# Optimization experiments

Hardware: AMD Instinct MI355X
Metric: run time of the kernel (lower is better)

## Reference

```python
import jax, jax.numpy as jnp
import numpy as np

# anchor encoding indices: [x,y,z,log w,log l,log h,sin,cos,vx,vy,vz]
NUM_HEADS = 8
LN_EPS = 1e-5


def layer_norm(x, g, b):
    mu = jnp.mean(x, axis=-1, keepdims=True)
    var = jnp.var(x, axis=-1, keepdims=True)
    return (x - mu) * jax.lax.rsqrt(var + LN_EPS) * g + b


def align_anchors_to_frame(anchor, Tm):
    # anchor: (..., N, 11), Tm: (..., 4, 4)
    R = Tm[..., :3, :3]
    t = Tm[..., :3, 3]
    center = jnp.einsum('...ij,...nj->...ni', R, anchor[..., 0:3]) + t[..., None, :]
    size = anchor[..., 3:6]
    yaw = jnp.einsum('...ij,...nj->...ni', R[..., :2, :2], anchor[..., 6:8])
    vel = jnp.einsum('...ij,...nj->...ni', R, anchor[..., 8:11])
    return jnp.concatenate([center, size, yaw, vel], axis=-1)


def setup_inputs() -> dict:
    key = jax.random.key(0)
    ks = jax.random.split(key, 12)
    B, T, N, C, E, A = 2, 12, 1024, 256, 256, 11
    inp = {
        'seq_features': jax.random.normal(ks[0], (B, T, N, C), jnp.float32),
        'seq_anchors': jax.random.normal(ks[1], (B, T, N, A), jnp.float32),
        'T_ego_his2cur': jax.random.normal(ks[2], (B, T, 4, 4), jnp.float32),
        'Wf': jax.random.normal(ks[3], (E, C), jnp.float32) * (C ** -0.5),
        'bf': jnp.zeros((E,), jnp.float32),
        'Wa': jax.random.normal(ks[4], (E, A), jnp.float32) * (A ** -0.5),
        'ba': jnp.zeros((E,), jnp.float32),
        'Win': jax.random.normal(ks[5], (3 * E, E), jnp.float32) * (E ** -0.5),
        'bin_': jnp.zeros((3 * E,), jnp.float32),
        'gamma': jnp.ones((E,), jnp.float32),
        'beta': jnp.zeros((E,), jnp.float32),
    }
    return inp


def reference(seq_features, seq_anchors, T_ego_his2cur, Wf, bf, Wa, ba, Win, bin_, gamma, beta):
    B, T, N, C = seq_features.shape
    E = gamma.shape[0]
    H = NUM_HEADS
    D = E // H

    feat_cur = seq_features[:, 1:]    # (B,T-1,N,C)
    feat_prev = seq_features[:, :-1]
    anc_cur = seq_anchors[:, 1:]
    anc_prev = align_anchors_to_frame(seq_anchors[:, :-1], T_ego_his2cur[:, 1:])

    tok_cur = layer_norm(feat_cur @ Wf.T + bf + anc_cur @ Wa.T + ba, gamma, beta)
    tok_prev = layer_norm(feat_prev @ Wf.T + bf + anc_prev @ Wa.T + ba, gamma, beta)

    Wq, Wk = Win[:E], Win[E:2 * E]
    bq, bk = bin_[:E], bin_[E:2 * E]
    scale = np.float32(D) ** np.float32(-0.5)
    q = ((tok_cur @ Wq.T + bq) * scale).reshape(B, T - 1, N, H, D)
    k = (tok_prev @ Wk.T + bk).reshape(B, T - 1, N, H, D)

    scores = jnp.einsum('btnhd,btmhd->bthnm', q, k)  # (B,T-1,H,N,N)
    attn = jax.nn.softmax(scores, axis=-1).mean(axis=2)  # head-averaged weights

    eye = jnp.broadcast_to(jnp.eye(N, dtype=seq_features.dtype), (B, 1, N, N))
    return jnp.concatenate([eye, attn], axis=1)  # (B,T,N,N)
```

## Files before the change

kernel.cpp:

```cpp
#include <hip/hip_runtime.h>
#include <hip/hip_bf16.h>
#include <math.h>

#define LN_EPS 1e-5f

typedef short bf16x8 __attribute__((ext_vector_type(8)));
typedef float f32x4 __attribute__((ext_vector_type(4)));

__device__ inline short f2bf(float f) {
  union { float f; unsigned u; } v; v.f = f;
  unsigned r = v.u + 0x7FFFu + ((v.u >> 16) & 1u);
  return (short)(r >> 16);
}
__device__ inline float bf2f(unsigned short s) {
  union { unsigned u; float f; } v; v.u = ((unsigned)s) << 16;
  return v.f;
}
__device__ inline float fast_exp2(float x) {
#if __has_builtin(__builtin_amdgcn_exp2f)
  return __builtin_amdgcn_exp2f(x);
#else
  return __expf(x * 0.69314718056f);
#endif
}

__global__ __launch_bounds__(256) void convert_kernel(const float* __restrict__ Wf,
    const float* __restrict__ Win, short* __restrict__ Wfb, short* __restrict__ Wqkb)
{
  size_t i = ((size_t)blockIdx.x * 256 + threadIdx.x) * 8;
  const float* src;
  short* dst;
  if (i < 65536) { src = Wf + i; dst = Wfb + i; }
  else { src = Win + (i - 65536); dst = Wqkb + (i - 65536); }
  f32x4 x0 = *(const f32x4*)src;
  f32x4 x1 = *(const f32x4*)(src + 4);
  bf16x8 v;
  v[0] = f2bf(x0[0]); v[1] = f2bf(x0[1]); v[2] = f2bf(x0[2]); v[3] = f2bf(x0[3]);
  v[4] = f2bf(x1[0]); v[5] = f2bf(x1[1]); v[6] = f2bf(x1[2]); v[7] = f2bf(x1[3]);
  *(bf16x8*)dst = v;
}

__global__ __launch_bounds__(256) void feat_ln(const float* __restrict__ Af,
    const short* __restrict__ Wb, const float* __restrict__ bfv,
    const float* __restrict__ anchors, const float* __restrict__ Tego,
    const float* __restrict__ Wa, const float* __restrict__ ba,
    const float* __restrict__ gamma, const float* __restrict__ beta,
    short* __restrict__ tok_cur, short* __restrict__ tok_prev)
{
  __shared__ short lda[64][40];
  __shared__ short ldb[256][40];
  __shared__ float aC[64][12];
  __shared__ float aP[64][12];
  const int tid = threadIdx.x;
  const int wid = tid >> 6, lane = tid & 63;
  const int quad = lane >> 4, l15 = lane & 15;
  const int row0 = blockIdx.x * 64;
  const int s24 = row0 >> 10;
  const int b = s24 / 12, t = s24 - b * 12;
  const int n0 = row0 & 1023;
  const int srow = tid >> 2, sseg = tid & 3;

  if (tid < 64) {
    const float* ap = anchors + ((size_t)s24 * 1024 + n0 + tid) * 11;
    float a[11];
    #pragma unroll
    for (int j = 0; j < 11; ++j) a[j] = ap[j];
    #pragma unroll
    for (int j = 0; j < 11; ++j) aC[tid][j] = a[j];
    if (t <= 10) {
      const float* Tm = Tego + ((size_t)b * 12 + t + 1) * 16;
      float r00 = Tm[0], r01 = Tm[1], r02 = Tm[2],  t0 = Tm[3];
      float r10 = Tm[4], r11 = Tm[5], r12 = Tm[6],  t1 = Tm[7];
      float r20 = Tm[8], r21 = Tm[9], r22 = Tm[10], t2 = Tm[11];
      aP[tid][0] = r00 * a[0] + r01 * a[1] + r02 * a[2] + t0;
      aP[tid][1] = r10 * a[0] + r11 * a[1] + r12 * a[2] + t1;
      aP[tid][2] = r20 * a[0] + r21 * a[1] + r22 * a[2] + t2;
      aP[tid][3] = a[3]; aP[tid][4] = a[4]; aP[tid][5] = a[5];
      aP[tid][6] = r00 * a[6] + r01 * a[7];
      aP[tid][7] = r10 * a[6] + r11 * a[7];
      aP[tid][8] = r00 * a[8] + r01 * a[9] + r02 * a[10];
      aP[tid][9] = r10 * a[8] + r11 * a[9] + r12 * a[10];
      aP[tid][10] = r20 * a[8] + r21 * a[9] + r22 * a[10];
    }
  }

  f32x4 z = {0.f, 0.f, 0.f, 0.f};
  f32x4 acc[16];
  #pragma unroll
  for (int j = 0; j < 16; ++j) acc[j] = z;

  const float* ap0 = Af + (size_t)(row0 + srow) * 256 + sseg * 8;
  const short* wp = Wb + (size_t)srow * 256 + sseg * 8;

  for (int kk = 0; kk < 256; kk += 32) {
    {
      f32x4 x0 = *(const f32x4*)(ap0 + kk);
      f32x4 x1 = *(const f32x4*)(ap0 + kk + 4);
      bf16x8 vv;
      vv[0] = f2bf(x0[0]); vv[1] = f2bf(x0[1]); vv[2] = f2bf(x0[2]); vv[3] = f2bf(x0[3]);
      vv[4] = f2bf(x1[0]); vv[5] = f2bf(x1[1]); vv[6] = f2bf(x1[2]); vv[7] = f2bf(x1[3]);
      *(bf16x8*)&lda[srow][sseg * 8] = vv;
    }
    #pragma unroll
    for (int p = 0; p < 4; ++p)
      *(bf16x8*)&ldb[srow + 64 * p][sseg * 8] =
          *(const bf16x8*)(wp + (size_t)p * 64 * 256 + kk);
    __syncthreads();
    bf16x8 af = *(const bf16x8*)&lda[wid * 16 + l15][quad * 8];
    #pragma unroll
    for (int j = 0; j < 16; ++j) {
      bf16x8 bq = *(const bf16x8*)&ldb[j * 16 + l15][quad * 8];
      acc[j] = __builtin_amdgcn_mfma_f32_16x16x32_bf16(af, bq, acc[j], 0, 0, 0);
    }
    __syncthreads();
  }

  float cb[16];
  #pragma unroll
  for (int j = 0; j < 16; ++j) {
    int col = j * 16 + l15;
    cb[j] = bfv[col] + ba[col];
  }

  auto emit = [&](const float (*aS)[12], short* dst, size_t tokbase) {
    float arow[4][11];
    #pragma unroll
    for (int r = 0; r < 4; ++r)
      #pragma unroll
      for (int jj = 0; jj < 11; ++jj)
        arow[r][jj] = aS[wid * 16 + quad * 4 + r][jj];
    float s1[4] = {0.f, 0.f, 0.f, 0.f};
    float s2[4] = {0.f, 0.f, 0.f, 0.f};
    #pragma unroll
    for (int j = 0; j < 16; ++j) {
      const float* war = Wa + (size_t)(j * 16 + l15) * 11;
      float wa[11];
      #pragma unroll
      for (int jj = 0; jj < 11; ++jj) wa[jj] = war[jj];
      #pragma unroll
      for (int r = 0; r < 4; ++r) {
        float d = 0.f;
        #pragma unroll
        for (int jj = 0; jj < 11; ++jj) d += wa[jj] * arow[r][jj];
        float v = acc[j][r] + cb[j] + d;
        s1[r] += v; s2[r] += v * v;
      }
    }
    #pragma unroll
    for (int r = 0; r < 4; ++r) {
      #pragma unroll
      for (int off = 1; off < 16; off <<= 1) {
        s1[r] += __shfl_xor(s1[r], off);
        s2[r] += __shfl_xor(s2[r], off);
      }
    }
    float mean[4], rstd[4];
    #pragma unroll
    for (int r = 0; r < 4; ++r) {
      mean[r] = s1[r] * (1.0f / 256.0f);
      float var = s2[r] * (1.0f / 256.0f) - mean[r] * mean[r];
      rstd[r] = rsqrtf(var + LN_EPS);
    }
    #pragma unroll
    for (int j = 0; j < 16; ++j) {
      int col = j * 16 + l15;
      const float* war = Wa + (size_t)col * 11;
      float wa[11];
      #pragma unroll
      for (int jj = 0; jj < 11; ++jj) wa[jj] = war[jj];
      float g = gamma[col], be = beta[col];
      #pragma unroll
      for (int r = 0; r < 4; ++r) {
        float d = 0.f;
        #pragma unroll
        for (int jj = 0; jj < 11; ++jj) d += wa[jj] * arow[r][jj];
        float v = acc[j][r] + cb[j] + d;
        int n = n0 + wid * 16 + quad * 4 + r;
        dst[(tokbase + n) * 256 + col] = f2bf((v - mean[r]) * rstd[r] * g + be);
      }
    }
  };

  if (t >= 1)  emit(aC, tok_cur,  (size_t)(b * 11 + t - 1) * 1024);
  if (t <= 10) emit(aP, tok_prev, (size_t)(b * 11 + t) * 1024);
}

__global__ __launch_bounds__(256) void gemm_qk(const short* __restrict__ tokc,
    const short* __restrict__ tokp, const short* __restrict__ Wqkb,
    const float* __restrict__ binv, short* __restrict__ qb, short* __restrict__ kb)
{
  const int sel = blockIdx.z;
  const short* Ap = sel ? tokp : tokc;
  const short* W = Wqkb + (size_t)sel * 65536;
  const float* bias = binv + sel * 256;
  const float alpha = sel ? 1.0f : 0.17677669529663687f * 1.4426950408889634f;
  short* Out = sel ? kb : qb;

  __shared__ short lda[128][40];
  __shared__ short ldb[128][40];
  const int tid = threadIdx.x;
  const int bm = blockIdx.x * 128, bn = blockIdx.y * 128;
  const int wid = tid >> 6, lane = tid & 63;
  const int quad = lane >> 4, l15 = lane & 15;
  const int wm = (wid & 1) * 64, wn = (wid >> 1) * 64;
  const int srow = tid >> 2, sseg = tid & 3;

  f32x4 z = {0.f, 0.f, 0.f, 0.f};
  f32x4 acc[4][4];
  #pragma unroll
  for (int i = 0; i < 4; ++i)
    #pragma unroll
    for (int j = 0; j < 4; ++j) acc[i][j] = z;

  const short* a0 = Ap + (size_t)(bm + srow) * 256 + sseg * 8;
  const short* a1 = Ap + (size_t)(bm + srow + 64) * 256 + sseg * 8;
  const short* b0 = W + (size_t)(bn + srow) * 256 + sseg * 8;
  const short* b1 = W + (size_t)(bn + srow + 64) * 256 + sseg * 8;

  for (int kk = 0; kk < 256; kk += 32) {
    *(bf16x8*)&lda[srow][sseg * 8]      = *(const bf16x8*)(a0 + kk);
    *(bf16x8*)&lda[srow + 64][sseg * 8] = *(const bf16x8*)(a1 + kk);
    *(bf16x8*)&ldb[srow][sseg * 8]      = *(const bf16x8*)(b0 + kk);
    *(bf16x8*)&ldb[srow + 64][sseg * 8] = *(const bf16x8*)(b1 + kk);
    __syncthreads();
    bf16x8 af[4], bq[4];
    #pragma unroll
    for (int i = 0; i < 4; ++i) {
      af[i] = *(const bf16x8*)&lda[wm + i * 16 + l15][quad * 8];
      bq[i] = *(const bf16x8*)&ldb[wn + i * 16 + l15][quad * 8];
    }
    #pragma unroll
    for (int i = 0; i < 4; ++i)
      #pragma unroll
      for (int j = 0; j < 4; ++j)
        acc[i][j] = __builtin_amdgcn_mfma_f32_16x16x32_bf16(af[i], bq[j], acc[i][j], 0, 0, 0);
    __syncthreads();
  }

  #pragma unroll
  for (int i = 0; i < 4; ++i)
    #pragma unroll
    for (int j = 0; j < 4; ++j)
      #pragma unroll
      for (int r = 0; r < 4; ++r) {
        int grow = bm + wm + i * 16 + quad * 4 + r;
        int gcol = bn + wn + j * 16 + l15;
        float v = (acc[i][j][r] + bias[gcol]) * alpha;
        int btr = grow >> 10, nn = grow & 1023, h = gcol >> 5, d = gcol & 31;
        Out[(((size_t)btr * 8 + h) * 1024 + nn) * 32 + d] = f2bf(v);
      }
}

__global__ __launch_bounds__(256) void denom_kernel(const short* __restrict__ q,
  const short* __restrict__ k, float* __restrict__ dinv)
{
  __shared__ short kst[2][4096];
  const int tid = threadIdx.x, wid = tid >> 6, lane = tid & 63;
  const int quad = lane >> 4, l15 = lane & 15;
  const int h = blockIdx.y, bt = blockIdx.z;
  const int n0 = blockIdx.x * 128 + wid * 32;
  const size_t base = ((size_t)bt * 8 + h) * 32768;
  bf16x8 qf0 = *(const bf16x8*)(q + base + (size_t)(n0 + l15) * 32 + quad * 8);
  bf16x8 qf1 = *(const bf16x8*)(q + base + (size_t)(n0 + 16 + l15) * 32 + quad * 8);
  const short* ksA = k + base + (size_t)(wid * 16) * 32 + lane * 8;
  const short* ksB = k + base + (size_t)((wid + 4) * 16) * 32 + lane * 8;
  const int wswz = ((lane & 3) ^ ((lane >> 3) & 3)) * 8;
  const int rswz = (quad ^ ((l15 >> 1) & 3)) * 8;
  short* lwA = &kst[0][wid * 512 + (lane >> 2) * 32 + wswz];
  short* lwB = &kst[0][(wid + 4) * 512 + (lane >> 2) * 32 + wswz];

  f32x4 z = {0.f, 0.f, 0.f, 0.f};
  float s0 = 0.f, s1 = 0.f;

  bf16x8 stA = *(const bf16x8*)ksA;
  bf16x8 stB = *(const bf16x8*)ksB;
  *(bf16x8*)lwA = stA;
  *(bf16x8*)lwB = stB;
  __syncthreads();

  #pragma unroll 1
  for (int rd = 0; rd < 8; ++rd) {
    const int buf = rd & 1;
    if (rd < 7) {
      stA = *(const bf16x8*)(ksA + (size_t)(rd + 1) * 128 * 32);
      stB = *(const bf16x8*)(ksB + (size_t)(rd + 1) * 128 * 32);
    }
    #pragma unroll
    for (int s = 0; s < 8; ++s) {
      bf16x8 kf = *(const bf16x8*)&kst[buf][s * 512 + l15 * 32 + rswz];
      f32x4 c0 = __builtin_amdgcn_mfma_f32_16x16x32_bf16(kf, qf0, z, 0, 0, 0);
      f32x4 c1 = __builtin_amdgcn_mfma_f32_16x16x32_bf16(kf, qf1, z, 0, 0, 0);
      s0 += fast_exp2(c0[0]) + fast_exp2(c0[1]) + fast_exp2(c0[2]) + fast_exp2(c0[3]);
      s1 += fast_exp2(c1[0]) + fast_exp2(c1[1]) + fast_exp2(c1[2]) + fast_exp2(c1[3]);
    }
    if (rd < 7) {
      *(bf16x8*)(lwA + ((buf ^ 1) << 12)) = stA;
      *(bf16x8*)(lwB + ((buf ^ 1) << 12)) = stB;
    }
    __syncthreads();
  }
  s0 += __shfl_xor(s0, 16); s0 += __shfl_xor(s0, 32);
  s1 += __shfl_xor(s1, 16); s1 += __shfl_xor(s1, 32);
  if (quad == 0) {
    float* dp = dinv + ((size_t)bt * 8 + h) * 1024 + n0;
    dp[l15] = 1.f / s0;
    dp[16 + l15] = 1.f / s1;
  }
}

__global__ __launch_bounds__(256) void prob_kernel(const short* __restrict__ q,
  const short* __restrict__ k, const float* __restrict__ dinv, float* __restrict__ out)
{
  __shared__ short kst[2][4096];
  const int tid = threadIdx.x, wid = tid >> 6, lane = tid & 63;
  const int quad = lane >> 4, l15 = lane & 15;
  const int bt = blockIdx.z;
  const int n0 = blockIdx.x * 128 + wid * 32;
  const int mbase = blockIdx.y * 128;
  const int b = bt / 11, t = bt - b * 11;

  bf16x8 qf0[8], qf1[8];
  float invd0[8], invd1[8];
  #pragma unroll
  for (int h = 0; h < 8; ++h) {
    const size_t base = ((size_t)bt * 8 + h) * 32768;
    qf0[h] = *(const bf16x8*)(q + base + (size_t)(n0 + l15) * 32 + quad * 8);
    qf1[h] = *(const bf16x8*)(q + base + (size_t)(n0 + 16 + l15) * 32 + quad * 8);
    invd0[h] = dinv[((size_t)bt * 8 + h) * 1024 + n0 + l15] * 0.125f;
    invd1[h] = dinv[((size_t)bt * 8 + h) * 1024 + n0 + 16 + l15] * 0.125f;
  }
  const short* ksA = k + (((size_t)bt * 8 + wid    ) * 1024 + mbase) * 32 + lane * 8;
  const short* ksB = k + (((size_t)bt * 8 + wid + 4) * 1024 + mbase) * 32 + lane * 8;
  const int wswz = ((lane & 3) ^ ((lane >> 3) & 3)) * 8;
  const int rswz = (quad ^ ((l15 >> 1) & 3)) * 8;
  short* lwA = &kst[0][wid * 512 + (lane >> 2) * 32 + wswz];
  short* lwB = &kst[0][(wid + 4) * 512 + (lane >> 2) * 32 + wswz];

  float* ob0 = out + ((size_t)(b * 12 + t + 1) * 1024 + n0 + l15) * 1024
                   + mbase + quad * 4;
  float* ob1 = ob0 + (size_t)16 * 1024;
  f32x4 z = {0.f, 0.f, 0.f, 0.f};

  bf16x8 stA = *(const bf16x8*)ksA;
  bf16x8 stB = *(const bf16x8*)ksB;
  *(bf16x8*)lwA = stA;
  *(bf16x8*)lwB = stB;
  __syncthreads();

  #pragma unroll 1
  for (int mt = 0; mt < 8; ++mt) {
    const int buf = mt & 1;
    if (mt < 7) {
      stA = *(const bf16x8*)(ksA + (size_t)(mt + 1) * 16 * 32);
      stB = *(const bf16x8*)(ksB + (size_t)(mt + 1) * 16 * 32);
    }
    f32x4 P0 = z, P1 = z;
    #pragma unroll
    for (int h = 0; h < 8; ++h) {
      bf16x8 kf = *(const bf16x8*)&kst[buf][h * 512 + l15 * 32 + rswz];
      f32x4 c0 = __builtin_amdgcn_mfma_f32_16x16x32_bf16(kf, qf0[h], z, 0, 0, 0);
      f32x4 c1 = __builtin_amdgcn_mfma_f32_16x16x32_bf16(kf, qf1[h], z, 0, 0, 0);
      #pragma unroll
      for (int r = 0; r < 4; ++r) {
        P0[r] += fast_exp2(c0[r]) * invd0[h];
        P1[r] += fast_exp2(c1[r]) * invd1[h];
      }
    }
    *(f32x4*)(ob0 + mt * 16) = P0;
    *(f32x4*)(ob1 + mt * 16) = P1;
    if (mt < 7) {
      *(bf16x8*)(lwA + ((buf ^ 1) << 12)) = stA;
      *(bf16x8*)(lwB + ((buf ^ 1) << 12)) = stB;
    }
    __syncthreads();
  }
}

__global__ __launch_bounds__(256) void eye_kernel(float* __restrict__ out) {
  int gid = blockIdx.x * 256 + threadIdx.x;
  int b = gid >> 18, rem = gid & 262143;
  int n = rem >> 8, m4 = rem & 255;
  f32x4 v = {0.f, 0.f, 0.f, 0.f};
  int c = n - m4 * 4;
  if (c >= 0 && c < 4) v[c] = 1.0f;
  *(f32x4*)(out + (size_t)b * 12582912 + (size_t)n * 1024 + m4 * 4) = v;
}

extern "C" void kernel_launch(void* const* d_in, const int* in_sizes, int n_in,
                              void* d_out, int out_size, void* d_ws, size_t ws_size,
                              hipStream_t stream)
{
  const float* sf   = (const float*)d_in[0];
  const float* sa   = (const float*)d_in[1];
  const float* te   = (const float*)d_in[2];
  const float* Wf   = (const float*)d_in[3];
  const float* bfv  = (const float*)d_in[4];
  const float* Wa   = (const float*)d_in[5];
  const float* ba   = (const float*)d_in[6];
  const float* Win  = (const float*)d_in[7];
  const float* binv = (const float*)d_in[8];
  const float* gam  = (const float*)d_in[9];
  const float* bet  = (const float*)d_in[10];
  float* out = (float*)d_out;

  char* w = (char*)d_ws;
  short* tok_cur  = (short*)w;  w += 11534336;
  short* tok_prev = (short*)w;  w += 11534336;
  short* qb       = (short*)w;  w += 11534336;
  short* kb       = (short*)w;  w += 11534336;
  float* dinv     = (float*)w;  w += 720896;
  short* Wfb      = (short*)w;  w += 131072;
  short* Wqkb     = (short*)w;  w += 262144;

  convert_kernel<<<dim3(96), 256, 0, stream>>>(Wf, Win, Wfb, Wqkb);
  feat_ln<<<dim3(384), 256, 0, stream>>>(sf, Wfb, bfv, sa, te, Wa, ba, gam, bet,
                                         tok_cur, tok_prev);
  gemm_qk<<<dim3(176, 2, 2), 256, 0, stream>>>(tok_cur, tok_prev, Wqkb, binv, qb, kb);
  denom_kernel<<<dim3(8, 8, 22), 256, 0, stream>>>(qb, kb, dinv);
  prob_kernel<<<dim3(8, 8, 22), 256, 0, stream>>>(qb, kb, dinv, out);
  eye_kernel<<<dim3(2048), 256, 0, stream>>>(out);
}
```

Before: 261.7 us.

## Split feat_ln into separate cur/prev blocks and stage Wa in LDS

Launches feat_ln with a second grid dimension so each block produces only tok_cur or tok_prev, doubling block count and dropping the serial double emit per block. Wa is staged into shared memory once per block, and the pre-LN values are kept in the accumulators so the anchor dot products are computed once instead of twice. The cost is that the feature GEMM is now recomputed by two blocks for most row tiles, roughly doubling feature reads and MFMA work in this stage.

After: 257.9 us. About the same (-1.4%).

```diff
diff --git a/kernel.cpp b/kernel.cpp
--- a/kernel.cpp
+++ b/kernel.cpp
@@ -47,41 +47,49 @@
     const float* __restrict__ gamma, const float* __restrict__ beta,
     short* __restrict__ tok_cur, short* __restrict__ tok_prev)
 {
+  const int which = blockIdx.y;
+  const int row0 = blockIdx.x * 64;
+  const int s24 = row0 >> 10;
+  const int b = s24 / 12, t = s24 - b * 12;
+  if (which == 0 && t == 0) return;
+  if (which == 1 && t == 11) return;
+
   __shared__ short lda[64][40];
   __shared__ short ldb[256][40];
-  __shared__ float aC[64][12];
-  __shared__ float aP[64][12];
+  __shared__ float ldWa[2816];
+  __shared__ float aS[64][12];
   const int tid = threadIdx.x;
   const int wid = tid >> 6, lane = tid & 63;
   const int quad = lane >> 4, l15 = lane & 15;
-  const int row0 = blockIdx.x * 64;
-  const int s24 = row0 >> 10;
-  const int b = s24 / 12, t = s24 - b * 12;
   const int n0 = row0 & 1023;
   const int srow = tid >> 2, sseg = tid & 3;
+
+  #pragma unroll
+  for (int i = 0; i < 11; ++i) ldWa[tid + i * 256] = Wa[tid + i * 256];
 
   if (tid < 64) {
     const float* ap = anchors + ((size_t)s24 * 1024 + n0 + tid) * 11;
     float a[11];
     #pragma unroll
     for (int j = 0; j < 11; ++j) a[j] = ap[j];
-    #pragma unroll
-    for (int j = 0; j < 11; ++j) aC[tid][j] = a[j];
-    if (t <= 10) {
+    if (which == 1) {
       const float* Tm = Tego + ((size_t)b * 12 + t + 1) * 16;
       float r00 = Tm[0], r01 = Tm[1], r02 = Tm[2],  t0 = Tm[3];
       float r10 = Tm[4], r11 = Tm[5], r12 = Tm[6],  t1 = Tm[7];
       float r20 = Tm[8], r21 = Tm[9], r22 = Tm[10], t2 = Tm[11];
-      aP[tid][0] = r00 * a[0] + r01 * a[1] + r02 * a[2] + t0;
-      aP[tid][1] = r10 * a[0] + r11 * a[1] + r12 * a[2] + t1;
-      aP[tid][2] = r20 * a[0] + r21 * a[1] + r22 * a[2] + t2;
-      aP[tid][3] = a[3]; aP[tid][4] = a[4]; aP[tid][5] = a[5];
-      aP[tid][6] = r00 * a[6] + r01 * a[7];
-      aP[tid][7] = r10 * a[6] + r11 * a[7];
-      aP[tid][8] = r00 * a[8] + r01 * a[9] + r02 * a[10];
-      aP[tid][9] = r10 * a[8] + r11 * a[9] + r12 * a[10];
-      aP[tid][10] = r20 * a[8] + r21 * a[9] + r22 * a[10];
-    }
+      float a0 = a[0], a1 = a[1], a2 = a[2];
+      float a6 = a[6], a7 = a[7], a8 = a[8], a9 = a[9], a10 = a[10];
+      a[0] = r00 * a0 + r01 * a1 + r02 * a2 + t0;
+      a[1] = r10 * a0 + r11 * a1 + r12 * a2 + t1;
+      a[2] = r20 * a0 + r21 * a1 + r22 * a2 + t2;
+      a[6] = r00 * a6 + r01 * a7;
+      a[7] = r10 * a6 + r11 * a7;
+      a[8] = r00 * a8 + r01 * a9 + r02 * a10;
+      a[9] = r10 * a8 + r11 * a9 + r12 * a10;
+      a[10] = r20 * a8 + r21 * a9 + r22 * a10;
+    }
+    #pragma unroll
+    for (int j = 0; j < 11; ++j) aS[tid][j] = a[j];
   }
 
   f32x4 z = {0.f, 0.f, 0.f, 0.f};
@@ -115,74 +123,61 @@
     __syncthreads();
   }
 
-  float cb[16];
+  float arow[4][11];
+  #pragma unroll
+  for (int r = 0; r < 4; ++r)
+    #pragma unroll
+    for (int jj = 0; jj < 11; ++jj)
+      arow[r][jj] = aS[wid * 16 + quad * 4 + r][jj];
+
+  float s1[4] = {0.f, 0.f, 0.f, 0.f};
+  float s2[4] = {0.f, 0.f, 0.f, 0.f};
   #pragma unroll
   for (int j = 0; j < 16; ++j) {
-    int col = j * 16 + l15;
-    cb[j] = bfv[col] + ba[col];
-  }
-
-  auto emit = [&](const float (*aS)[12], short* dst, size_t tokbase) {
-    float arow[4][11];
-    #pragma unroll
-    for (int r = 0; r < 4; ++r)
+    const int col = j * 16 + l15;
+    const float cb = bfv[col] + ba[col];
+    float wa[11];
+    #pragma unroll
+    for (int jj = 0; jj < 11; ++jj) wa[jj] = ldWa[col * 11 + jj];
+    #pragma unroll
+    for (int r = 0; r < 4; ++r) {
+      float d = 0.f;
       #pragma unroll
-      for (int jj = 0; jj < 11; ++jj)
-        arow[r][jj] = aS[wid * 16 + quad * 4 + r][jj];
-    float s1[4] = {0.f, 0.f, 0.f, 0.f};
-    float s2[4] = {0.f, 0.f, 0.f, 0.f};
-    #pragma unroll
-    for (int j = 0; j < 16; ++j) {
-      const float* war = Wa + (size_t)(j * 16 + l15) * 11;
-      float wa[11];
-      #pragma unroll
-      for (int jj = 0; jj < 11; ++jj) wa[jj] = war[jj];
-      #pragma unroll
-      for (int r = 0; r < 4; ++r) {
-        float d = 0.f;
-        #pragma unroll
-        for (int jj = 0; jj < 11; ++jj) d += wa[jj] * arow[r][jj];
-        float v = acc[j][r] + cb[j] + d;
-        s1[r] += v; s2[r] += v * v;
-      }
-    }
+      for (int jj = 0; jj < 11; ++jj) d += wa[jj] * arow[r][jj];
+      float v = acc[j][r] + cb + d;
+      acc[j][r] = v;
+      s1[r] += v; s2[r] += v * v;
+    }
+  }
+  #pragma unroll
+  for (int r = 0; r < 4; ++r) {
+    #pragma unroll
+    for (int off = 1; off < 16; off <<= 1) {
+      s1[r] += __shfl_xor(s1[r], off);
+      s2[r] += __shfl_xor(s2[r], off);
+    }
+  }
+  float mean[4], rstd[4];
+  #pragma unroll
+  for (int r = 0; r < 4; ++r) {
+    mean[r] = s1[r] * (1.0f / 256.0f);
+    float var = s2[r] * (1.0f / 256.0f) - mean[r] * mean[r];
+    rstd[r] = rsqrtf(var + LN_EPS);
+  }
+
+  short* dst = which ? tok_prev : tok_cur;
+  const size_t tokbase = which ? (size_t)(b * 11 + t) * 1024
+                               : (size_t)(b * 11 + t - 1) * 1024;
+  #pragma unroll
+  for (int j = 0; j < 16; ++j) {
+    const int col = j * 16 + l15;
+    const float g = gamma[col], be = beta[col];
     #pragma unroll
     for (int r = 0; r < 4; ++r) {
-      #pragma unroll
-      for (int off = 1; off < 16; off <<= 1) {
-        s1[r] += __shfl_xor(s1[r], off);
-        s2[r] += __shfl_xor(s2[r], off);
-      }
-    }
-    float mean[4], rstd[4];
-    #pragma unroll
-    for (int r = 0; r < 4; ++r) {
-      mean[r] = s1[r] * (1.0f / 256.0f);
-      float var = s2[r] * (1.0f / 256.0f) - mean[r] * mean[r];
-      rstd[r] = rsqrtf(var + LN_EPS);
-    }
-    #pragma unroll
-    for (int j = 0; j < 16; ++j) {
-      int col = j * 16 + l15;
-      const float* war = Wa + (size_t)col * 11;
-      float wa[11];
-      #pragma unroll
-      for (int jj = 0; jj < 11; ++jj) wa[jj] = war[jj];
-      float g = gamma[col], be = beta[col];
-      #pragma unroll
-      for (int r = 0; r < 4; ++r) {
-        float d = 0.f;
-        #pragma unroll
-        for (int jj = 0; jj < 11; ++jj) d += wa[jj] * arow[r][jj];
-        float v = acc[j][r] + cb[j] + d;
-        int n = n0 + wid * 16 + quad * 4 + r;
-        dst[(tokbase + n) * 256 + col] = f2bf((v - mean[r]) * rstd[r] * g + be);
-      }
-    }
-  };
-
-  if (t >= 1)  emit(aC, tok_cur,  (size_t)(b * 11 + t - 1) * 1024);
-  if (t <= 10) emit(aP, tok_prev, (size_t)(b * 11 + t) * 1024);
+      const int n = n0 + wid * 16 + quad * 4 + r;
+      dst[(tokbase + n) * 256 + col] = f2bf((acc[j][r] - mean[r]) * rstd[r] * g + be);
+    }
+  }
 }
 
 __global__ __launch_bounds__(256) void gemm_qk(const short* __restrict__ tokc,
@@ -413,8 +408,8 @@
   short* Wqkb     = (short*)w;  w += 262144;
 
   convert_kernel<<<dim3(96), 256, 0, stream>>>(Wf, Win, Wfb, Wqkb);
-  feat_ln<<<dim3(384), 256, 0, stream>>>(sf, Wfb, bfv, sa, te, Wa, ba, gam, bet,
-                                         tok_cur, tok_prev);
+  feat_ln<<<dim3(384, 2), 256, 0, stream>>>(sf, Wfb, bfv, sa, te, Wa, ba, gam, bet,
+                                            tok_cur, tok_prev);
   gemm_qk<<<dim3(176, 2, 2), 256, 0, stream>>>(tok_cur, tok_prev, Wqkb, binv, qb, kb);
   denom_kernel<<<dim3(8, 8, 22), 256, 0, stream>>>(qb, kb, dinv);
   prob_kernel<<<dim3(8, 8, 22), 256, 0, stream>>>(qb, kb, dinv, out);
```
